# Kernel optimization log

Measured on AMD Instinct MI355X. Metric: run time of the kernel, lower is better.

Reference implementation:

```python
import jax, jax.numpy as jnp
import numpy as np

BN_EPS = 1e-5
L2_EPS = 1e-8


def l2norm(x, axis=-1):
    # matches torch: x / (sqrt(sum(x^2)) + eps)
    n = jnp.sqrt(jnp.sum(x * x, axis=axis, keepdims=True)) + L2_EPS
    return x / n


def setup_inputs() -> dict:
    key = jax.random.key(0)
    ks = jax.random.split(key, 8)
    B, N, D, E = 512, 193, 512, 2048
    g = 4                      # uniform pid-group size (<= max_rows=8)
    k_tok = (N - 1) // 2       # = 96, matches DynamicLinearProjection k
    H = E // 2                 # MLP hidden = 1024
    base_features = jax.random.normal(ks[0], (B, N, D), jnp.float32)
    atten = jax.random.uniform(ks[1], (B, N, N), jnp.float32)
    pid = jnp.arange(B) // g   # contiguous groups of size g
    # dynamic projection params for group size g
    W_dyn = jax.random.normal(ks[2], (g, D), jnp.float32)          # weights[f'weight_{g}'] ~ randn
    b_dyn = jnp.zeros((g,), jnp.float32)
    W_lin = jax.random.normal(ks[3], (E, k_tok * g), jnp.float32) * 0.02  # linears[f'linear_{g}']
    b_lin = jnp.zeros((E,), jnp.float32)
    # MLP(input=512, hidden=1024, output=2048, 2 layers)
    W1 = jax.random.normal(ks[4], (H, D), jnp.float32) * 0.02
    b1 = jnp.zeros((H,), jnp.float32)
    gamma1 = jnp.ones((H,), jnp.float32)
    beta1 = jnp.zeros((H,), jnp.float32)
    W2 = jax.random.normal(ks[5], (E, H), jnp.float32) * 0.02
    b2 = jnp.zeros((E,), jnp.float32)
    return {"base_features": base_features, "atten": atten, "pid": pid,
            "W_dyn": W_dyn, "b_dyn": b_dyn, "W_lin": W_lin, "b_lin": b_lin,
            "W1": W1, "b1": b1, "gamma1": gamma1, "beta1": beta1,
            "W2": W2, "b2": b2}


def reference(base_features, atten, pid, W_dyn, b_dyn, W_lin, b_lin,
              W1, b1, gamma1, beta1, W2, b2):
    B, N, D = base_features.shape
    k_tok = (N - 1) // 2                      # 96
    g = W_dyn.shape[0]                        # uniform group size (pid = arange//g)
    G = B // g
    E = W_lin.shape[0]
    # --- top-k token selection (atten[:, :, 0] = -1, then topk over atten[:, 0, :]) ---
    scores = atten[:, 0, :].at[:, 0].set(-1.0)            # (B, N)
    _, idx = jax.lax.top_k(scores, k_tok)                 # (B, k_tok), descending
    feats = jnp.take_along_axis(base_features, idx[:, :, None], axis=1)  # (B, k_tok, D)
    # --- per-pid-group dynamic projection (uniform groups -> one batched GEMM) ---
    # torch: cat group members -> (g*k_tok, D); F.linear(x, W_dyn, b_dyn).T -> (g, g*k_tok); linear_g -> (g, E)
    Xg = feats.reshape(G, g * k_tok, D)
    y = jnp.einsum('gnd,rd->grn', Xg, W_dyn) + b_dyn[None, :, None]     # (G, g, g*k_tok)
    new_feats = jnp.einsum('gri,oi->gro', y, W_lin) + b_lin             # (G, g, E)
    # scatter: output[member_idx] = row; contiguous groups => plain reshape
    new_feats = l2norm(new_feats.reshape(B, E))
    # --- MLP branch on l2-normalized selected features ---
    x = l2norm(feats).reshape(B * k_tok, D)
    h = x @ W1.T + b1
    mu = jnp.mean(h, axis=0)
    var = jnp.var(h, axis=0)                  # biased, as torch BN training-mode
    h = (h - mu) * jax.lax.rsqrt(var + BN_EPS) * gamma1 + beta1
    h = jax.nn.relu(h)
    out = (h @ W2.T + b2).reshape(B, k_tok, E)
    pooled = jnp.max(out, axis=1)             # maxk_pool1d_var with k=1 => max over tokens
    return (pooled + new_feats).astype(jnp.float32)
```

## Files before the change

### kernel.cpp

```cpp
#include <hip/hip_runtime.h>
#include <math.h>

#define B_   512
#define N_   193
#define D_   512
#define E_   2048
#define KTOK 96
#define H_   1024
#define M1   (B_ * KTOK)
#define KGD  (KTOK * 4)

typedef _Float16 half8 __attribute__((ext_vector_type(8)));
typedef _Float16 half4v __attribute__((ext_vector_type(4)));
typedef float floatx4 __attribute__((ext_vector_type(4)));

__device__ __forceinline__ void gll16(const _Float16* g, _Float16* l) {
    __builtin_amdgcn_global_load_lds(
        (const __attribute__((address_space(1))) unsigned int*)(const void*)g,
        (__attribute__((address_space(3))) unsigned int*)(void*)l, 16, 0, 0);
}

__global__ void zero_stats_kernel(double* stats) {
    int i = blockIdx.x * 256 + threadIdx.x;
    if (i < 2 * H_) stats[i] = 0.0;
}

__global__ void topk_kernel(const float* __restrict__ atten, int* __restrict__ idx) {
    __shared__ float s[N_];
    int b = blockIdx.x;
    const float* row = atten + (size_t)b * N_ * N_;
    for (int i = threadIdx.x; i < N_; i += blockDim.x)
        s[i] = (i == 0) ? -1.0f : row[i];
    __syncthreads();
    for (int i = threadIdx.x; i < N_; i += blockDim.x) {
        float v = s[i];
        int rank = 0;
        for (int j = 0; j < N_; ++j) {
            float u = s[j];
            rank += (u > v) || (u == v && j < i);
        }
        if (rank < KTOK) idx[b * KTOK + rank] = i;
    }
}

__global__ __launch_bounds__(256) void gather_kernel(
        const float* __restrict__ base, const int* __restrict__ idx,
        const float* __restrict__ W_dyn, const float* __restrict__ b_dyn,
        _Float16* __restrict__ Xh, float* __restrict__ Y) {
    int ln = threadIdx.x & 63, wv = threadIdx.x >> 6;
    int rowid = blockIdx.x * 4 + wv;
    int b = rowid / KTOK, t = rowid - b * KTOK;
    int tok = idx[rowid];
    const float4* src = (const float4*)(base + ((size_t)b * N_ + tok) * D_);
    float4 v0 = src[ln * 2], v1 = src[ln * 2 + 1];

    float vals[5];
    vals[0] = v0.x * v0.x + v0.y * v0.y + v0.z * v0.z + v0.w * v0.w
            + v1.x * v1.x + v1.y * v1.y + v1.z * v1.z + v1.w * v1.w;
#pragma unroll
    for (int r = 0; r < 4; ++r) {
        const float4* wr = (const float4*)(W_dyn + r * D_);
        float4 w0 = wr[ln * 2], w1 = wr[ln * 2 + 1];
        vals[1 + r] = v0.x * w0.x + v0.y * w0.y + v0.z * w0.z + v0.w * w0.w
                    + v1.x * w1.x + v1.y * w1.y + v1.z * w1.z + v1.w * w1.w;
    }
#pragma unroll
    for (int c = 0; c < 5; ++c)
#pragma unroll
        for (int o = 32; o > 0; o >>= 1) vals[c] += __shfl_xor(vals[c], o, 64);

    float inv = 1.0f / (sqrtf(vals[0]) + 1e-8f);
    half8 o8;
    o8[0] = (_Float16)(v0.x * inv); o8[1] = (_Float16)(v0.y * inv);
    o8[2] = (_Float16)(v0.z * inv); o8[3] = (_Float16)(v0.w * inv);
    o8[4] = (_Float16)(v1.x * inv); o8[5] = (_Float16)(v1.y * inv);
    o8[6] = (_Float16)(v1.z * inv); o8[7] = (_Float16)(v1.w * inv);
    *(half8*)&Xh[(size_t)rowid * D_ + ln * 8] = o8;
    if (ln == 0) {
        int g = b >> 2;
        int n = (b & 3) * KTOK + t;
#pragma unroll
        for (int r = 0; r < 4; ++r)
            Y[(size_t)(g * 4 + r) * KGD + n] = vals[1 + r] + b_dyn[r];
    }
}

__global__ __launch_bounds__(256) void newfeat_kernel(
        const float* __restrict__ Y, const float* __restrict__ W_lin,
        const float* __restrict__ b_lin, float* __restrict__ NF) {
    __shared__ float sy[4][KGD];
    __shared__ float red[4][4];
    __shared__ float tot[4];
    int b0 = blockIdx.x * 4;
    int tid = threadIdx.x;
    for (int l = tid; l < 4 * KGD; l += 256)
        sy[l / KGD][l % KGD] = Y[(size_t)b0 * KGD + l];
    __syncthreads();

    float out[4][8];
    float ssq[4] = {0.f, 0.f, 0.f, 0.f};
#pragma unroll
    for (int q = 0; q < 8; ++q) {
        int o = tid + 256 * q;
        float a0 = 0.f, a1 = 0.f, a2 = 0.f, a3 = 0.f;
        const float4* wr = (const float4*)(W_lin + (size_t)o * KGD);
        for (int i4 = 0; i4 < KGD / 4; ++i4) {
            float4 w  = wr[i4];
            float4 s0 = *(const float4*)&sy[0][i4 * 4];
            float4 s1 = *(const float4*)&sy[1][i4 * 4];
            float4 s2 = *(const float4*)&sy[2][i4 * 4];
            float4 s3 = *(const float4*)&sy[3][i4 * 4];
            a0 += w.x * s0.x + w.y * s0.y + w.z * s0.z + w.w * s0.w;
            a1 += w.x * s1.x + w.y * s1.y + w.z * s1.z + w.w * s1.w;
            a2 += w.x * s2.x + w.y * s2.y + w.z * s2.z + w.w * s2.w;
            a3 += w.x * s3.x + w.y * s3.y + w.z * s3.z + w.w * s3.w;
        }
        float bl = b_lin[o];
        out[0][q] = a0 + bl; out[1][q] = a1 + bl;
        out[2][q] = a2 + bl; out[3][q] = a3 + bl;
#pragma unroll
        for (int r = 0; r < 4; ++r) ssq[r] += out[r][q] * out[r][q];
    }

    int lane = tid & 63, wid = tid >> 6;
#pragma unroll
    for (int c = 0; c < 4; ++c) {
        float v = ssq[c];
        for (int o = 32; o > 0; o >>= 1) v += __shfl_down(v, o, 64);
        if (lane == 0) red[c][wid] = v;
    }
    __syncthreads();
    if (tid < 4) tot[tid] = red[tid][0] + red[tid][1] + red[tid][2] + red[tid][3];
    __syncthreads();
#pragma unroll
    for (int r = 0; r < 4; ++r) {
        float norm = sqrtf(tot[r]) + 1e-8f;
#pragma unroll
        for (int q = 0; q < 8; ++q) {
            int o = tid + 256 * q;
            NF[(size_t)(b0 + r) * E_ + o] = out[r][q] / norm;
        }
    }
}

__global__ __launch_bounds__(256) void convw_kernel(
        const float* __restrict__ W1, const float* __restrict__ W2,
        _Float16* __restrict__ W1h, _Float16* __restrict__ W2h) {
    int i = blockIdx.x * 256 + threadIdx.x;
    if (i < 131072) {
        float4 v = *(const float4*)&W1[(size_t)i * 4];
        half4v o = {(_Float16)v.x, (_Float16)v.y, (_Float16)v.z, (_Float16)v.w};
        *(half4v*)&W1h[(size_t)i * 4] = o;
    } else {
        int j = i - 131072;
        float4 v = *(const float4*)&W2[(size_t)j * 4];
        half4v o = {(_Float16)v.x, (_Float16)v.y, (_Float16)v.z, (_Float16)v.w};
        *(half4v*)&W2h[(size_t)j * 4] = o;
    }
}


__global__ __launch_bounds__(512, 2) void gemm1s(
        const _Float16* __restrict__ A, const _Float16* __restrict__ Bm,
        const float* __restrict__ bias, _Float16* __restrict__ Cf16,
        double* __restrict__ stats) {
    constexpr int KA = 512, NS = 16, NBX = 4;
    __shared__ _Float16 Sl[4][14336];
    int tid = threadIdx.x;
    int ln = tid & 63, w = tid >> 6;
    int wr = w >> 2, wc = w & 3;
    int rid = blockIdx.x;
    int q = rid >> 3;
    int bx = q & (NBX - 1);
    int by = ((q / NBX) << 3) | (rid & 7);
    int n0 = bx * 256, m0 = by * 192;

    bool isA = (w < 4);
    const _Float16* sg[4];
    int ld[4];
    if (isA) {
#pragma unroll
        for (int i = 0; i < 3; ++i) {
            int j = w * 3 + i;
            int u = j * 64 + ln;
            int kg = u / 192, row = u - kg * 192;
            sg[i] = A + (size_t)(m0 + row) * KA + kg * 8;
            ld[i] = j * 512;
        }
        sg[3] = sg[0]; ld[3] = ld[0];
    } else {
#pragma unroll
        for (int i = 0; i < 4; ++i) {
            int j = (w - 4) * 4 + i;
            int u = j * 64 + ln;
            int kg = u >> 8, col = u & 255;
            sg[i] = Bm + (size_t)(n0 + col) * KA + kg * 8;
            ld[i] = 6144 + j * 512;
        }
    }

#define CSTAGE(s) { int ko = (s) * 32; _Float16* dst = &Sl[(s) & 3][0];        \
    if (isA) { gll16(sg[0] + ko, dst + ld[0]); gll16(sg[1] + ko, dst + ld[1]); \
               gll16(sg[2] + ko, dst + ld[2]); }                               \
    else     { gll16(sg[0] + ko, dst + ld[0]); gll16(sg[1] + ko, dst + ld[1]); \
               gll16(sg[2] + ko, dst + ld[2]); gll16(sg[3] + ko, dst + ld[3]); } }
#define WAITV(na, nb) { if (isA) asm volatile("s_waitcnt vmcnt(" #na ")" ::: "memory"); \
                        else     asm volatile("s_waitcnt vmcnt(" #nb ")" ::: "memory"); }

    int aofs[6], bofs[4];
#pragma unroll
    for (int f = 0; f < 6; ++f)
        aofs[f] = ((ln >> 4) * 192 + wr * 96 + f * 16 + (ln & 15)) * 8;
#pragma unroll
    for (int n = 0; n < 4; ++n)
        bofs[n] = 6144 + ((ln >> 4) * 256 + wc * 64 + n * 16 + (ln & 15)) * 8;

    floatx4 zero = {0.f, 0.f, 0.f, 0.f};
    floatx4 acc[6][4];
#pragma unroll
    for (int i = 0; i < 6; ++i)
#pragma unroll
        for (int j = 0; j < 4; ++j) acc[i][j] = zero;

    CSTAGE(0); CSTAGE(1); CSTAGE(2);
    WAITV(6, 8);
    __builtin_amdgcn_s_barrier();

    for (int s = 0; s < NS; ++s) {
        const _Float16* SL = &Sl[s & 3][0];
        half8 bv[4], av[6];
#pragma unroll
        for (int n = 0; n < 4; ++n) bv[n] = *(const half8*)&SL[bofs[n]];
#pragma unroll
        for (int f = 0; f < 6; ++f) av[f] = *(const half8*)&SL[aofs[f]];
        if (s + 3 < NS) CSTAGE(s + 3);
        __builtin_amdgcn_sched_barrier(0);
        asm volatile("s_waitcnt lgkmcnt(0)" ::: "memory");
        __builtin_amdgcn_sched_barrier(0);
        __builtin_amdgcn_s_setprio(1);
#pragma unroll
        for (int f = 0; f < 6; ++f)
#pragma unroll
            for (int n = 0; n < 4; ++n)
                acc[f][n] = __builtin_amdgcn_mfma_f32_16x16x32_f16(av[f], bv[n], acc[f][n], 0, 0, 0);
        __builtin_amdgcn_s_setprio(0);
        __builtin_amdgcn_sched_barrier(0);
        if (s + 1 < NS) {
            if (s + 3 < NS)      { WAITV(6, 8); }
            else if (s + 2 < NS) { WAITV(3, 4); }
            else                 { WAITV(0, 0); }
        }
        __builtin_amdgcn_s_barrier();
    }
#undef CSTAGE
#undef WAITV

    float cs[4] = {0.f, 0.f, 0.f, 0.f}, cq[4] = {0.f, 0.f, 0.f, 0.f};
#pragma unroll
    for (int f = 0; f < 6; ++f) {
        int row = m0 + wr * 96 + f * 16 + (ln >> 4) * 4;
#pragma unroll
        for (int n = 0; n < 4; ++n) {
            int col = n0 + wc * 64 + n * 16 + (ln & 15);
            float bb = bias[col];
#pragma unroll
            for (int r = 0; r < 4; ++r) {
                float v = acc[f][n][r] + bb;
                Cf16[(size_t)(row + r) * H_ + col] = (_Float16)v;
                cs[n] += v; cq[n] += v * v;
            }
        }
    }
#pragma unroll
    for (int n = 0; n < 4; ++n) {
        cs[n] += __shfl_xor(cs[n], 16); cs[n] += __shfl_xor(cs[n], 32);
        cq[n] += __shfl_xor(cq[n], 16); cq[n] += __shfl_xor(cq[n], 32);
    }
    float* sp = (float*)&Sl[0][0];
    __syncthreads();
    if (ln < 16) {
#pragma unroll
        for (int n = 0; n < 4; ++n) {
            int c = wc * 64 + n * 16 + ln;
            sp[(wr * 256 + c) * 2 + 0] = cs[n];
            sp[(wr * 256 + c) * 2 + 1] = cq[n];
        }
    }
    __syncthreads();
    if (tid < 256) {
        float s0 = sp[tid * 2]     + sp[(256 + tid) * 2];
        float q0 = sp[tid * 2 + 1] + sp[(256 + tid) * 2 + 1];
        atomicAdd(&stats[n0 + tid], (double)s0);
        atomicAdd(&stats[H_ + n0 + tid], (double)q0);
    }
}

__global__ void finalize_kernel(const double* __restrict__ stats,
                                const float* __restrict__ gamma,
                                const float* __restrict__ beta,
                                _Float16* __restrict__ scsh16) {
    int c = blockIdx.x * 256 + threadIdx.x;
    if (c >= H_) return;
    double mean = stats[c] / (double)M1;
    double var  = stats[H_ + c] / (double)M1 - mean * mean;
    float sc = gamma[c] * (float)(1.0 / sqrt(var + 1e-5));
    float sh = beta[c] - (float)mean * sc;
    scsh16[c] = (_Float16)sc;
    scsh16[H_ + c] = (_Float16)sh;
}

__device__ __forceinline__ half8 bnrelu8(half8 h, const _Float16* scp, const _Float16* shp) {
    half8 s = *(const half8*)scp, t = *(const half8*)shp, o;
#pragma unroll
    for (int e = 0; e < 8; ++e) {
        float v = (float)h[e] * (float)s[e] + (float)t[e];
        o[e] = (_Float16)fmaxf(v, 0.f);
    }
    return o;
}

__global__ __launch_bounds__(512, 2) void gemm2f(
        const _Float16* __restrict__ Hb, const _Float16* __restrict__ Bm,
        const _Float16* __restrict__ scsh16, const float* __restrict__ bias,
        const float* __restrict__ NF, float* __restrict__ out) {
    constexpr int KA = 1024, NS = 32, NBX = 8;
    __shared__ _Float16 Sl[4][14336];
    __shared__ _Float16 scL[H_], shL[H_];
    int tid = threadIdx.x;
    int ln = tid & 63, w = tid >> 6;
    int wr = w >> 2, wc = w & 3;
    int rid = blockIdx.x;
    int qq = rid >> 3;
    int bx = qq & (NBX - 1);
    int by = ((qq / NBX) << 3) | (rid & 7);
    int n0 = bx * 256, m0 = by * 192;
    bool isA = (w < 4);

    for (int i = tid; i < H_; i += 512) { scL[i] = scsh16[i]; shL[i] = scsh16[H_ + i]; }

    const _Float16 *sgA0 = Hb, *sgA1 = Hb, *sgA2 = Hb;
    int ldA0 = 0, ldA1 = 0, ldA2 = 0, kgA0 = 0, kgA1 = 0, kgA2 = 0;
    const _Float16* sgB[4] = {Bm, Bm, Bm, Bm};
    int ldB[4] = {6144, 6144, 6144, 6144};
    if (isA) {
        { int j = w * 3 + 0; int u = j * 64 + ln; kgA0 = u / 192; int row = u - kgA0 * 192;
          sgA0 = Hb + (size_t)(m0 + row) * KA + kgA0 * 8; ldA0 = j * 512; }
        { int j = w * 3 + 1; int u = j * 64 + ln; kgA1 = u / 192; int row = u - kgA1 * 192;
          sgA1 = Hb + (size_t)(m0 + row) * KA + kgA1 * 8; ldA1 = j * 512; }
        { int j = w * 3 + 2; int u = j * 64 + ln; kgA2 = u / 192; int row = u - kgA2 * 192;
          sgA2 = Hb + (size_t)(m0 + row) * KA + kgA2 * 8; ldA2 = j * 512; }
    } else {
#pragma unroll
        for (int i = 0; i < 4; ++i) {
            int j = (w - 4) * 4 + i;
            int u = j * 64 + ln;
            int kg = u >> 8, col = u & 255;
            sgB[i] = Bm + (size_t)(n0 + col) * KA + kg * 8;
            ldB[i] = 6144 + j * 512;
        }
    }

#define A_ISSUE(t, Ra, Rb, Rc) { Ra = *(const half8*)(sgA0 + (size_t)(t) * 32); \
    Rb = *(const half8*)(sgA1 + (size_t)(t) * 32);                              \
    Rc = *(const half8*)(sgA2 + (size_t)(t) * 32); }
#define A_XFRM(t, Ra, Rb, Rc) { _Float16* dst = &Sl[(t) & 3][0]; int c0 = (t) * 32; \
    *(half8*)(dst + ldA0 + ln * 8) = bnrelu8(Ra, &scL[c0 + kgA0 * 8], &shL[c0 + kgA0 * 8]); \
    *(half8*)(dst + ldA1 + ln * 8) = bnrelu8(Rb, &scL[c0 + kgA1 * 8], &shL[c0 + kgA1 * 8]); \
    *(half8*)(dst + ldA2 + ln * 8) = bnrelu8(Rc, &scL[c0 + kgA2 * 8], &shL[c0 + kgA2 * 8]); }
#define B_STAGE(t) { int ko = (t) * 32; _Float16* dst = &Sl[(t) & 3][0]; \
    gll16(sgB[0] + ko, dst + ldB[0]); gll16(sgB[1] + ko, dst + ldB[1]); \
    gll16(sgB[2] + ko, dst + ldB[2]); gll16(sgB[3] + ko, dst + ldB[3]); }

    int aofs[6], bofs[4];
#pragma unroll
    for (int f = 0; f < 6; ++f)
        aofs[f] = ((ln >> 4) * 192 + wr * 96 + f * 16 + (ln & 15)) * 8;
#pragma unroll
    for (int n = 0; n < 4; ++n)
        bofs[n] = 6144 + ((ln >> 4) * 256 + wc * 64 + n * 16 + (ln & 15)) * 8;

    floatx4 zero = {0.f, 0.f, 0.f, 0.f};
    floatx4 acc[6][4];
#pragma unroll
    for (int i = 0; i < 6; ++i)
#pragma unroll
        for (int j = 0; j < 4; ++j) acc[i][j] = zero;

    half8 e0a, e0b, e0c, e1a, e1b, e1c;

    if (isA) { A_ISSUE(0, e0a, e0b, e0c); A_ISSUE(1, e1a, e1b, e1c); }
    else     { B_STAGE(0); B_STAGE(1); B_STAGE(2); }
    asm volatile("s_waitcnt lgkmcnt(0)" ::: "memory");
    __builtin_amdgcn_s_barrier();
    if (isA) {
        A_XFRM(0, e0a, e0b, e0c);
        A_ISSUE(2, e0a, e0b, e0c);
        A_XFRM(1, e1a, e1b, e1c);
    } else {
        asm volatile("s_waitcnt vmcnt(8)" ::: "memory");
    }
    asm volatile("s_waitcnt lgkmcnt(0)" ::: "memory");
    __builtin_amdgcn_s_barrier();

#define SLOT(s, Ia, Ib, Ic, Xa, Xb, Xc) {                                       \
    const _Float16* SL = &Sl[(s) & 3][0];                                       \
    half8 bv[4], av[6];                                                         \
    _Pragma("unroll") for (int n = 0; n < 4; ++n) bv[n] = *(const half8*)&SL[bofs[n]]; \
    _Pragma("unroll") for (int f = 0; f < 6; ++f) av[f] = *(const half8*)&SL[aofs[f]]; \
    if ((s) + 3 < NS) { if (isA) { A_ISSUE((s) + 3, Ia, Ib, Ic); } else { B_STAGE((s) + 3); } } \
    __builtin_amdgcn_sched_barrier(0);                                          \
    asm volatile("s_waitcnt lgkmcnt(0)" ::: "memory");                          \
    __builtin_amdgcn_sched_barrier(0);                                          \
    __builtin_amdgcn_s_setprio(1);                                              \
    _Pragma("unroll") for (int f = 0; f < 6; ++f)                               \
        _Pragma("unroll") for (int n = 0; n < 4; ++n)                           \
            acc[f][n] = __builtin_amdgcn_mfma_f32_16x16x32_f16(av[f], bv[n], acc[f][n], 0, 0, 0); \
    __builtin_amdgcn_s_setprio(0);                                              \
    __builtin_amdgcn_sched_barrier(0);                                          \
    if (isA) {                                                                  \
        if ((s) + 2 < NS) { A_XFRM((s) + 2, Xa, Xb, Xc); }                      \
        asm volatile("s_waitcnt lgkmcnt(0)" ::: "memory");                      \
    } else {                                                                    \
        if ((s) + 3 < NS)      { asm volatile("s_waitcnt vmcnt(8)" ::: "memory"); } \
        else if ((s) + 2 < NS) { asm volatile("s_waitcnt vmcnt(4)" ::: "memory"); } \
        else if ((s) + 1 < NS) { asm volatile("s_waitcnt vmcnt(0)" ::: "memory"); } \
    }                                                                           \
    __builtin_amdgcn_s_barrier();                                               \
}

    for (int s = 0; s < NS; s += 2) {
        SLOT(s,     e1a, e1b, e1c, e0a, e0b, e0c);
        SLOT(s + 1, e0a, e0b, e0c, e1a, e1b, e1c);
    }
#undef SLOT
#undef A_ISSUE
#undef A_XFRM
#undef B_STAGE

    int batch = by * 2 + wr;
#pragma unroll
    for (int n = 0; n < 4; ++n) {
        float m = -3.4e38f;
#pragma unroll
        for (int f = 0; f < 6; ++f)
#pragma unroll
            for (int r = 0; r < 4; ++r) m = fmaxf(m, acc[f][n][r]);
        m = fmaxf(m, __shfl_xor(m, 16));
        m = fmaxf(m, __shfl_xor(m, 32));
        if (ln < 16) {
            int col = n0 + wc * 64 + n * 16 + ln;
            out[(size_t)batch * E_ + col] = m + bias[col] + NF[(size_t)batch * E_ + col];
        }
    }
}

extern "C" void kernel_launch(void* const* d_in, const int* in_sizes, int n_in,
                              void* d_out, int out_size, void* d_ws, size_t ws_size,
                              hipStream_t stream) {
    (void)in_sizes; (void)n_in; (void)out_size; (void)ws_size;
    const float* base  = (const float*)d_in[0];
    const float* atten = (const float*)d_in[1];
    const float* W_dyn = (const float*)d_in[3];
    const float* b_dyn = (const float*)d_in[4];
    const float* W_lin = (const float*)d_in[5];
    const float* b_lin = (const float*)d_in[6];
    const float* W1    = (const float*)d_in[7];
    const float* b1    = (const float*)d_in[8];
    const float* gamma = (const float*)d_in[9];
    const float* beta  = (const float*)d_in[10];
    const float* W2    = (const float*)d_in[11];
    const float* b2    = (const float*)d_in[12];
    float* out = (float*)d_out;

    char* wsp = (char*)d_ws;
    int*      idx    = (int*)(wsp);
    float*    Y      = (float*)(wsp + 196608);
    float*    NF     = (float*)(wsp + 983040);
    double*   stats  = (double*)(wsp + 5177344);
    _Float16* scsh16 = (_Float16*)(wsp + 5193728);
    _Float16* W1h    = (_Float16*)(wsp + 5201920);
    _Float16* W2h    = (_Float16*)(wsp + 6250496);
    _Float16* Xh     = (_Float16*)(wsp + 10444800);
    _Float16* Hbh    = (_Float16*)(wsp + 60776448);

    zero_stats_kernel<<<8, 256, 0, stream>>>(stats);
    topk_kernel<<<B_, 256, 0, stream>>>(atten, idx);
    convw_kernel<<<2560, 256, 0, stream>>>(W1, W2, W1h, W2h);
    gather_kernel<<<M1 / 4, 256, 0, stream>>>(base, idx, W_dyn, b_dyn, Xh, Y);
    newfeat_kernel<<<B_ / 4, 256, 0, stream>>>(Y, W_lin, b_lin, NF);
    gemm1s<<<1024, 512, 0, stream>>>(Xh, W1h, b1, Hbh, stats);
    finalize_kernel<<<4, 256, 0, stream>>>(stats, gamma, beta, scsh16);
    gemm2f<<<2048, 512, 0, stream>>>(Hbh, W2h, scsh16, b2, NF, out);
}
```

Before: 539.8 us.

## Split gemm2f LDS into separate A/B ring buffers with shallower prefetch

Replaces the four-stage shared LDS ring in the second GEMM with a three-slot B buffer and a double-buffered A buffer, and reduces prefetch depth from three to two stages. The launch bound is raised to request four blocks per CU. The intent is to cut LDS footprint so more blocks can be resident. The cost is less latency hiding and tighter register limits that may cause spills.

```diff
diff --git a/kernel.cpp b/kernel.cpp
--- a/kernel.cpp
+++ b/kernel.cpp
@@ -159,7 +159,6 @@
     }
 }
 
-
 __global__ __launch_bounds__(512, 2) void gemm1s(
         const _Float16* __restrict__ A, const _Float16* __restrict__ Bm,
         const float* __restrict__ bias, _Float16* __restrict__ Cf16,
@@ -319,12 +318,13 @@
     return o;
 }
 
-__global__ __launch_bounds__(512, 2) void gemm2f(
+__global__ __launch_bounds__(512, 4) void gemm2f(
         const _Float16* __restrict__ Hb, const _Float16* __restrict__ Bm,
         const _Float16* __restrict__ scsh16, const float* __restrict__ bias,
         const float* __restrict__ NF, float* __restrict__ out) {
     constexpr int KA = 1024, NS = 32, NBX = 8;
-    __shared__ _Float16 Sl[4][14336];
+    __shared__ _Float16 Bsl[3][8192];
+    __shared__ _Float16 Asl[2][6144];
     __shared__ _Float16 scL[H_], shL[H_];
     int tid = threadIdx.x;
     int ln = tid & 63, w = tid >> 6;
@@ -341,7 +341,7 @@
     const _Float16 *sgA0 = Hb, *sgA1 = Hb, *sgA2 = Hb;
     int ldA0 = 0, ldA1 = 0, ldA2 = 0, kgA0 = 0, kgA1 = 0, kgA2 = 0;
     const _Float16* sgB[4] = {Bm, Bm, Bm, Bm};
-    int ldB[4] = {6144, 6144, 6144, 6144};
+    int ldB[4] = {0, 0, 0, 0};
     if (isA) {
         { int j = w * 3 + 0; int u = j * 64 + ln; kgA0 = u / 192; int row = u - kgA0 * 192;
           sgA0 = Hb + (size_t)(m0 + row) * KA + kgA0 * 8; ldA0 = j * 512; }
@@ -356,18 +356,18 @@
             int u = j * 64 + ln;
             int kg = u >> 8, col = u & 255;
             sgB[i] = Bm + (size_t)(n0 + col) * KA + kg * 8;
-            ldB[i] = 6144 + j * 512;
+            ldB[i] = j * 512;
         }
     }
 
 #define A_ISSUE(t, Ra, Rb, Rc) { Ra = *(const half8*)(sgA0 + (size_t)(t) * 32); \
     Rb = *(const half8*)(sgA1 + (size_t)(t) * 32);                              \
     Rc = *(const half8*)(sgA2 + (size_t)(t) * 32); }
-#define A_XFRM(t, Ra, Rb, Rc) { _Float16* dst = &Sl[(t) & 3][0]; int c0 = (t) * 32; \
+#define A_XFRM(t, Ra, Rb, Rc) { _Float16* dst = &Asl[(t) & 1][0]; int c0 = (t) * 32; \
     *(half8*)(dst + ldA0 + ln * 8) = bnrelu8(Ra, &scL[c0 + kgA0 * 8], &shL[c0 + kgA0 * 8]); \
     *(half8*)(dst + ldA1 + ln * 8) = bnrelu8(Rb, &scL[c0 + kgA1 * 8], &shL[c0 + kgA1 * 8]); \
     *(half8*)(dst + ldA2 + ln * 8) = bnrelu8(Rc, &scL[c0 + kgA2 * 8], &shL[c0 + kgA2 * 8]); }
-#define B_STAGE(t) { int ko = (t) * 32; _Float16* dst = &Sl[(t) & 3][0]; \
+#define B_STAGE(t, sl) { int ko = (t) * 32; _Float16* dst = &Bsl[sl][0]; \
     gll16(sgB[0] + ko, dst + ldB[0]); gll16(sgB[1] + ko, dst + ldB[1]); \
     gll16(sgB[2] + ko, dst + ldB[2]); gll16(sgB[3] + ko, dst + ldB[3]); }
 
@@ -377,7 +377,7 @@
         aofs[f] = ((ln >> 4) * 192 + wr * 96 + f * 16 + (ln & 15)) * 8;
 #pragma unroll
     for (int n = 0; n < 4; ++n)
-        bofs[n] = 6144 + ((ln >> 4) * 256 + wc * 64 + n * 16 + (ln & 15)) * 8;
+        bofs[n] = ((ln >> 4) * 256 + wc * 64 + n * 16 + (ln & 15)) * 8;
 
     floatx4 zero = {0.f, 0.f, 0.f, 0.f};
     floatx4 acc[6][4];
@@ -389,25 +389,25 @@
     half8 e0a, e0b, e0c, e1a, e1b, e1c;
 
     if (isA) { A_ISSUE(0, e0a, e0b, e0c); A_ISSUE(1, e1a, e1b, e1c); }
-    else     { B_STAGE(0); B_STAGE(1); B_STAGE(2); }
+    else     { B_STAGE(0, 0); B_STAGE(1, 1); }
     asm volatile("s_waitcnt lgkmcnt(0)" ::: "memory");
     __builtin_amdgcn_s_barrier();
-    if (isA) {
-        A_XFRM(0, e0a, e0b, e0c);
-        A_ISSUE(2, e0a, e0b, e0c);
-        A_XFRM(1, e1a, e1b, e1c);
-    } else {
-        asm volatile("s_waitcnt vmcnt(8)" ::: "memory");
-    }
+    if (isA) { A_XFRM(0, e0a, e0b, e0c); }
+    else     { asm volatile("s_waitcnt vmcnt(4)" ::: "memory"); }
     asm volatile("s_waitcnt lgkmcnt(0)" ::: "memory");
     __builtin_amdgcn_s_barrier();
 
+    int bb = 0;
 #define SLOT(s, Ia, Ib, Ic, Xa, Xb, Xc) {                                       \
-    const _Float16* SL = &Sl[(s) & 3][0];                                       \
+    const _Float16* SB = &Bsl[bb][0];                                           \
+    const _Float16* SA = &Asl[(s) & 1][0];                                      \
     half8 bv[4], av[6];                                                         \
-    _Pragma("unroll") for (int n = 0; n < 4; ++n) bv[n] = *(const half8*)&SL[bofs[n]]; \
-    _Pragma("unroll") for (int f = 0; f < 6; ++f) av[f] = *(const half8*)&SL[aofs[f]]; \
-    if ((s) + 3 < NS) { if (isA) { A_ISSUE((s) + 3, Ia, Ib, Ic); } else { B_STAGE((s) + 3); } } \
+    _Pragma("unroll") for (int n = 0; n < 4; ++n) bv[n] = *(const half8*)&SB[bofs[n]]; \
+    _Pragma("unroll") for (int f = 0; f < 6; ++f) av[f] = *(const half8*)&SA[aofs[f]]; \
+    if ((s) + 2 < NS) {                                                         \
+        if (isA) { A_ISSUE((s) + 2, Ia, Ib, Ic); }                              \
+        else { int bs = bb + 2 - ((bb >= 1) ? 3 : 0); B_STAGE((s) + 2, bs); }   \
+    }                                                                           \
     __builtin_amdgcn_sched_barrier(0);                                          \
     asm volatile("s_waitcnt lgkmcnt(0)" ::: "memory");                          \
     __builtin_amdgcn_sched_barrier(0);                                          \
@@ -418,19 +418,19 @@
     __builtin_amdgcn_s_setprio(0);                                              \
     __builtin_amdgcn_sched_barrier(0);                                          \
     if (isA) {                                                                  \
-        if ((s) + 2 < NS) { A_XFRM((s) + 2, Xa, Xb, Xc); }                      \
+        if ((s) + 1 < NS) { A_XFRM((s) + 1, Xa, Xb, Xc); }                      \
         asm volatile("s_waitcnt lgkmcnt(0)" ::: "memory");                      \
     } else {                                                                    \
-        if ((s) + 3 < NS)      { asm volatile("s_waitcnt vmcnt(8)" ::: "memory"); } \
-        else if ((s) + 2 < NS) { asm volatile("s_waitcnt vmcnt(4)" ::: "memory"); } \
+        if ((s) + 2 < NS)      { asm volatile("s_waitcnt vmcnt(4)" ::: "memory"); } \
         else if ((s) + 1 < NS) { asm volatile("s_waitcnt vmcnt(0)" ::: "memory"); } \
     }                                                                           \
     __builtin_amdgcn_s_barrier();                                               \
+    bb = (bb == 2) ? 0 : bb + 1;                                                \
 }
 
     for (int s = 0; s < NS; s += 2) {
-        SLOT(s,     e1a, e1b, e1c, e0a, e0b, e0c);
-        SLOT(s + 1, e0a, e0b, e0c, e1a, e1b, e1c);
+        SLOT(s,     e0a, e0b, e0c, e1a, e1b, e1c);
+        SLOT(s + 1, e1a, e1b, e1c, e0a, e0b, e0c);
     }
 #undef SLOT
 #undef A_ISSUE
```

New measurement: 1.661 ms. 3.08x slower.
